# Kernel optimization log

Measured on AMD Instinct MI355X. Metric: run time of the kernel, lower is better.

Reference implementation:

```python
import jax, jax.numpy as jnp
import numpy as np

K = 5  # spline kernel size per pseudo-coordinate dim (dim=2 -> 25 weight matrices)


def spline_conv(x, pseudo, W, root, bias, tails, heads):
    # x: [N, Cin], pseudo: [E, 2] in [0,1], W: [K*K, Cin, Cout], root: [Cin, Cout], bias: [Cout]
    # Degree-1 open B-spline basis: each dim contributes 2 taps -> 4 (basis, weight-index) pairs per edge.
    N = x.shape[0]
    v = pseudo * (K - 1)                         # [E, 2]
    f = jnp.minimum(jnp.floor(v), K - 2)         # clamp so idx+1 <= K-1 (pseudo==1 edge case)
    frac = v - f                                 # [E, 2]
    fi = f.astype(jnp.int32)
    # Precompute per-node transform under every kernel bin: Z[n, k, :] = x[n] @ W[k]
    Z = jnp.einsum('ni,kio->nko', x, W)          # [N, 25, Cout]
    msg = jnp.zeros((pseudo.shape[0], W.shape[2]), x.dtype)
    for s in range(4):                           # 4 basis combos (static small loop)
        b0, b1 = s & 1, (s >> 1) & 1
        basis = (frac[:, 0] if b0 else 1.0 - frac[:, 0]) * (frac[:, 1] if b1 else 1.0 - frac[:, 1])
        wi = (fi[:, 0] + b0) + (fi[:, 1] + b1) * K   # [E] flattened kernel index
        msg = msg + basis[:, None] * Z[tails, wi]    # gather transformed source feature
    agg = jax.ops.segment_max(msg, heads, num_segments=N)  # scatter-max at target nodes
    agg = jnp.where(jnp.isfinite(agg), agg, 0.0)            # empty segments -> 0 (torch_scatter semantics)
    return agg + x @ root + bias


def setup_inputs() -> dict:
    N, E, D = 4096, 65536, 1024
    key = jax.random.key(0)
    ks = jax.random.split(key, 12)
    descs = jax.random.normal(ks[0], (N, D), dtype=jnp.float32)
    pts = jax.random.uniform(ks[1], (N, 2), dtype=jnp.float32) * 256.0  # keypoint coords, rescale=256 in source
    tails = jax.random.randint(ks[2], (E,), 0, N)
    heads = jax.random.randint(ks[3], (E,), 0, N)
    W1 = jax.random.normal(ks[4], (K * K, D, D), dtype=jnp.float32) * 0.02
    root1 = jax.random.normal(ks[5], (D, D), dtype=jnp.float32) * 0.03
    bias1 = jnp.zeros((D,), dtype=jnp.float32)
    W2 = jax.random.normal(ks[6], (K * K, D, D), dtype=jnp.float32) * 0.02
    root2 = jax.random.normal(ks[7], (D, D), dtype=jnp.float32) * 0.03
    bias2 = jnp.zeros((D,), dtype=jnp.float32)
    return {"descs": descs, "pts": pts, "W1": W1, "root1": root1, "bias1": bias1,
            "W2": W2, "root2": root2, "bias2": bias2, "tails": tails, "heads": heads}


def reference(descs, pts, W1, root1, bias1, W2, root2, bias2, tails, heads):
    # Edge pseudo-coordinates: 0.5*(pts[tail]-pts[head])/256 + 0.5, clipped to [0,1] (Net.to_pyg_graph)
    pseudo = jnp.clip(0.5 * (pts[tails] - pts[heads]) / 256.0 + 0.5, 0.0, 1.0)
    # SConv: relu(conv1) -> conv2, then residual x + 0.1*result (SiameseSConvOnNodes)
    h1 = jax.nn.relu(spline_conv(descs, pseudo, W1, root1, bias1, tails, heads))
    h2 = spline_conv(h1, pseudo, W2, root2, bias2, tails, heads)
    return descs + 0.1 * h2
```

## Files before the change

### kernel.cpp

```cpp
#include <hip/hip_runtime.h>
#include <hip/hip_bf16.h>
#include <math.h>


#define DN 4096
#define DE 65536
#define DF 1024
#define NMAT 26
#define NCOLS (NMAT * DF)

typedef __attribute__((ext_vector_type(8))) short short8;
typedef __attribute__((ext_vector_type(4))) float f32x4;
typedef unsigned long long ull;

__device__ __forceinline__ float bf2f(unsigned short u) {
    return __uint_as_float(((unsigned int)u) << 16);
}
__device__ __forceinline__ unsigned short f2bf(float f) {
    unsigned int x = __float_as_uint(f);
    x += 0x7fffu + ((x >> 16) & 1u);
    return (unsigned short)(x >> 16);
}
__device__ __forceinline__ void gld16(const unsigned short* g, unsigned short* l) {
    __builtin_amdgcn_global_load_lds(
        (const __attribute__((address_space(1))) unsigned int*)g,
        (__attribute__((address_space(3))) unsigned int*)l, 16, 0, 0);
}

__global__ void k_convert_x(const float* __restrict__ x, unsigned short* __restrict__ xb) {
    int i = (blockIdx.x * blockDim.x + threadIdx.x) * 4;
    float4 v = *(const float4*)(x + i);
    union { unsigned short u[4]; ull ll; } o;
    o.u[0] = f2bf(v.x); o.u[1] = f2bf(v.y); o.u[2] = f2bf(v.z); o.u[3] = f2bf(v.w);
    *(ull*)(xb + i) = o.ll;
}

__global__ void k_hist(const int* __restrict__ heads, int* __restrict__ cnt) {
    int e = blockIdx.x * blockDim.x + threadIdx.x;
    atomicAdd(&cnt[heads[e]], 1);
}

__global__ __launch_bounds__(1024)
void k_scan(const int* __restrict__ cnt, int* __restrict__ row_off, int* __restrict__ cursor) {
    __shared__ int part[1024];
    int tid = threadIdx.x;
    int base = tid * 4;
    int v[4], s = 0;
#pragma unroll
    for (int j = 0; j < 4; ++j) { v[j] = s; s += cnt[base + j]; }
    part[tid] = s;
    __syncthreads();
    for (int off = 1; off < 1024; off <<= 1) {
        int t = (tid >= off) ? part[tid - off] : 0;
        __syncthreads();
        part[tid] += t;
        __syncthreads();
    }
    int excl = (tid == 0) ? 0 : part[tid - 1];
#pragma unroll
    for (int j = 0; j < 4; ++j) {
        row_off[base + j] = excl + v[j];
        cursor[base + j]  = excl + v[j];
    }
    if (tid == 1023) row_off[4096] = part[1023];
}

__global__ void k_scatter(const float* __restrict__ pts,
                          const int* __restrict__ tails, const int* __restrict__ heads,
                          int* __restrict__ cursor,
                          int2* __restrict__ ei, float4* __restrict__ eb) {
    int e = blockIdx.x * blockDim.x + threadIdx.x;
    int t = tails[e], h = heads[e];
    float ptx = pts[2 * t], pty = pts[2 * t + 1];
    float phx = pts[2 * h], phy = pts[2 * h + 1];
    float p0 = fminf(fmaxf((ptx - phx) * (0.5f / 256.f) + 0.5f, 0.f), 1.f);
    float p1 = fminf(fmaxf((pty - phy) * (0.5f / 256.f) + 0.5f, 0.f), 1.f);
    float v0 = p0 * 4.f, v1 = p1 * 4.f;
    float f0 = fminf(floorf(v0), 3.f), f1 = fminf(floorf(v1), 3.f);
    float fr0 = v0 - f0, fr1 = v1 - f1;
    int i0 = (int)f0, i1 = (int)f1;
    int wi0 = i0 + i1 * 5;
    int wi1 = wi0 + 1;
    int wi2 = wi0 + 5;
    int wi3 = wi0 + 6;
    float4 b;
    b.x = (1.f - fr0) * (1.f - fr1);
    b.y = fr0 * (1.f - fr1);
    b.z = (1.f - fr0) * fr1;
    b.w = fr0 * fr1;
    int pos = atomicAdd(&cursor[h], 1);
    ei[pos] = make_int2(t, wi0 | (wi1 << 8) | (wi2 << 16) | (wi3 << 24));
    eb[pos] = b;
}

__global__ void k_transpose_w(const float* __restrict__ W, const float* __restrict__ root,
                              unsigned short* __restrict__ Wbt) {
    __shared__ float tile[64][65];
    int mat = blockIdx.z;
    const float* src = (mat < 25) ? (W + (size_t)mat * DF * DF) : root;
    unsigned short* dst = Wbt + (size_t)mat * DF * DF;
    int i0 = blockIdx.x * 64;
    int o0 = blockIdx.y * 64;
    int tx = threadIdx.x & 63, ty = threadIdx.x >> 6;
#pragma unroll
    for (int j = 0; j < 16; ++j) {
        int r = j * 4 + ty;
        tile[r][tx] = src[(size_t)(i0 + r) * DF + o0 + tx];
    }
    __syncthreads();
#pragma unroll
    for (int j = 0; j < 16; ++j) {
        int c = j * 4 + ty;
        dst[(size_t)(o0 + c) * DF + i0 + tx] = f2bf(tile[tx][c]);
    }
}

__global__ __launch_bounds__(256)
void k_gemm(const unsigned short* __restrict__ A,
            const unsigned short* __restrict__ B,
            unsigned short* __restrict__ C)
{
    __shared__ unsigned short As[128 * 32];
    __shared__ unsigned short Bs[128 * 32];
    const int tid = threadIdx.x;
    const int w = tid >> 6, ln = tid & 63;
    const int wr = w >> 1, wc = w & 1;
    const int bm = blockIdx.x, bn = blockIdx.y;

    f32x4 acc[4][4];
#pragma unroll
    for (int m = 0; m < 4; ++m)
#pragma unroll
        for (int n = 0; n < 4; ++n) acc[m][n] = (f32x4){0.f, 0.f, 0.f, 0.f};

    const size_t abase = (size_t)bm * 128 * 1024;
    const size_t bbase = (size_t)bn * 128 * 1024;
    const int k0 = (ln >> 4) * 8;
    const int rsel = ln & 15;

    for (int kk = 0; kk < 32; ++kk) {
        const int kbase = kk * 32;
#pragma unroll
        for (int j = 0; j < 2; ++j) {
            int chunk = j * 4 + w;
            int byteoff = chunk * 1024 + ln * 16;
            int row = byteoff >> 6;
            int ke = (byteoff & 63) >> 1;
            gld16(A + abase + (size_t)row * 1024 + kbase + ke, &As[chunk * 512]);
            gld16(B + bbase + (size_t)row * 1024 + kbase + ke, &Bs[chunk * 512]);
        }
        __syncthreads();
        short8 af[4], bf[4];
#pragma unroll
        for (int m = 0; m < 4; ++m)
            af[m] = *(const short8*)&As[(wr * 64 + m * 16 + rsel) * 32 + k0];
#pragma unroll
        for (int n = 0; n < 4; ++n)
            bf[n] = *(const short8*)&Bs[(wc * 64 + n * 16 + rsel) * 32 + k0];
#pragma unroll
        for (int m = 0; m < 4; ++m)
#pragma unroll
            for (int n = 0; n < 4; ++n)
                acc[m][n] = __builtin_amdgcn_mfma_f32_16x16x32_bf16(af[m], bf[n], acc[m][n], 0, 0, 0);
        __syncthreads();
    }

    const int r0 = (ln >> 4) * 4;
#pragma unroll
    for (int m = 0; m < 4; ++m) {
#pragma unroll
        for (int n = 0; n < 4; ++n) {
            int row = bm * 128 + wr * 64 + m * 16 + r0;
            int col = bn * 128 + wc * 64 + n * 16 + (ln & 15);
#pragma unroll
            for (int r = 0; r < 4; ++r)
                C[(size_t)(row + r) * NCOLS + col] = f2bf(acc[m][n][r]);
        }
    }
}

template <int LAYER>
__global__ __launch_bounds__(256)
void k_agg(const int* __restrict__ row_off,
           const int2* __restrict__ ei, const float4* __restrict__ eb,
           const unsigned short* __restrict__ Z,
           const float* __restrict__ bias,
           const float* __restrict__ descs,
           unsigned short* __restrict__ h1b, float* __restrict__ out)
{
    __shared__ int2  sei[64];
    __shared__ float4 seb[64];
    const int n = blockIdx.x;
    const int tid = threadIdx.x;
    const int d = tid * 4;
    const int s0 = row_off[n], s1 = row_off[n + 1];

    float vm0 = -3.3e38f, vm1 = -3.3e38f, vm2 = -3.3e38f, vm3 = -3.3e38f;

    for (int chunk = s0; chunk < s1; chunk += 64) {
        int cnum = min(64, s1 - chunk);
        if (tid < cnum) { sei[tid] = ei[chunk + tid]; seb[tid] = eb[chunk + tid]; }
        __syncthreads();
        for (int j = 0; j < cnum; ++j) {
            int2 ep = sei[j];
            float4 b = seb[j];
            const unsigned short* zt = Z + (size_t)ep.x * NCOLS + d;
            int w = ep.y;
            ull q0 = *(const ull*)(zt + ((w      ) & 255) * DF);
            ull q1 = *(const ull*)(zt + ((w >> 8 ) & 255) * DF);
            ull q2 = *(const ull*)(zt + ((w >> 16) & 255) * DF);
            ull q3 = *(const ull*)(zt + ((w >> 24) & 255) * DF);
            float m0 = b.x * bf2f((unsigned short)q0) + b.y * bf2f((unsigned short)q1)
                     + b.z * bf2f((unsigned short)q2) + b.w * bf2f((unsigned short)q3);
            float m1 = b.x * bf2f((unsigned short)(q0 >> 16)) + b.y * bf2f((unsigned short)(q1 >> 16))
                     + b.z * bf2f((unsigned short)(q2 >> 16)) + b.w * bf2f((unsigned short)(q3 >> 16));
            float m2 = b.x * bf2f((unsigned short)(q0 >> 32)) + b.y * bf2f((unsigned short)(q1 >> 32))
                     + b.z * bf2f((unsigned short)(q2 >> 32)) + b.w * bf2f((unsigned short)(q3 >> 32));
            float m3 = b.x * bf2f((unsigned short)(q0 >> 48)) + b.y * bf2f((unsigned short)(q1 >> 48))
                     + b.z * bf2f((unsigned short)(q2 >> 48)) + b.w * bf2f((unsigned short)(q3 >> 48));
            vm0 = fmaxf(vm0, m0); vm1 = fmaxf(vm1, m1);
            vm2 = fmaxf(vm2, m2); vm3 = fmaxf(vm3, m3);
        }
        __syncthreads();
    }
    if (s1 == s0) { vm0 = vm1 = vm2 = vm3 = 0.f; }

    const unsigned short* zr = Z + (size_t)n * NCOLS + 25 * DF + d;
    ull qr = *(const ull*)zr;
    float z0 = bf2f((unsigned short)qr),         z1 = bf2f((unsigned short)(qr >> 16));
    float z2 = bf2f((unsigned short)(qr >> 32)), z3 = bf2f((unsigned short)(qr >> 48));
    float b0 = bias[d], b1 = bias[d + 1], b2 = bias[d + 2], b3 = bias[d + 3];
    size_t o = (size_t)n * DF + d;
    if (LAYER == 1) {
        union { unsigned short u[4]; ull ll; } ov;
        ov.u[0] = f2bf(fmaxf(vm0 + z0 + b0, 0.f));
        ov.u[1] = f2bf(fmaxf(vm1 + z1 + b1, 0.f));
        ov.u[2] = f2bf(fmaxf(vm2 + z2 + b2, 0.f));
        ov.u[3] = f2bf(fmaxf(vm3 + z3 + b3, 0.f));
        *(ull*)(h1b + o) = ov.ll;
    } else {
        float4 dv = *(const float4*)(descs + o);
        float4 r;
        r.x = dv.x + 0.1f * (vm0 + z0 + b0);
        r.y = dv.y + 0.1f * (vm1 + z1 + b1);
        r.z = dv.z + 0.1f * (vm2 + z2 + b2);
        r.w = dv.w + 0.1f * (vm3 + z3 + b3);
        *(float4*)(out + o) = r;
    }
}

extern "C" void kernel_launch(void* const* d_in, const int* in_sizes, int n_in,
                              void* d_out, int out_size, void* d_ws, size_t ws_size,
                              hipStream_t stream) {
    const float* descs = (const float*)d_in[0];
    const float* pts   = (const float*)d_in[1];
    const float* W1    = (const float*)d_in[2];
    const float* root1 = (const float*)d_in[3];
    const float* bias1 = (const float*)d_in[4];
    const float* W2    = (const float*)d_in[5];
    const float* root2 = (const float*)d_in[6];
    const float* bias2 = (const float*)d_in[7];
    const int* tails   = (const int*)d_in[8];
    const int* heads   = (const int*)d_in[9];
    float* out = (float*)d_out;

    char* ws = (char*)d_ws;
    unsigned short* Wbt = (unsigned short*)ws;  ws += (size_t)NMAT * DF * DF * 2;
    unsigned short* xb  = (unsigned short*)ws;  ws += (size_t)DN * DF * 2;
    unsigned short* h1b = (unsigned short*)ws;  ws += (size_t)DN * DF * 2;
    unsigned short* Z   = (unsigned short*)ws;  ws += (size_t)DN * NCOLS * 2;
    int*  cnt     = (int*)ws;   ws += DN * 4;
    int*  row_off = (int*)ws;   ws += (DN + 1) * 4 + 4;
    int*  cursor  = (int*)ws;   ws += DN * 4;
    int2* ei      = (int2*)ws;  ws += (size_t)DE * 8;
    float4* eb    = (float4*)ws; ws += (size_t)DE * 16;

    hipMemsetAsync(cnt, 0, DN * 4, stream);
    k_convert_x<<<DN * DF / 4 / 256, 256, 0, stream>>>(descs, xb);
    k_hist<<<DE / 256, 256, 0, stream>>>(heads, cnt);
    k_scan<<<1, 1024, 0, stream>>>(cnt, row_off, cursor);
    k_scatter<<<DE / 256, 256, 0, stream>>>(pts, tails, heads, cursor, ei, eb);

    k_transpose_w<<<dim3(16, 16, NMAT), 256, 0, stream>>>(W1, root1, Wbt);
    k_gemm<<<dim3(DN / 128, NCOLS / 128), 256, 0, stream>>>(xb, Wbt, Z);
    k_agg<1><<<DN, 256, 0, stream>>>(row_off, ei, eb, Z, bias1, nullptr, h1b, nullptr);

    k_transpose_w<<<dim3(16, 16, NMAT), 256, 0, stream>>>(W2, root2, Wbt);
    k_gemm<<<dim3(DN / 128, NCOLS / 128), 256, 0, stream>>>(h1b, Wbt, Z);
    k_agg<2><<<DN, 256, 0, stream>>>(row_off, ei, eb, Z, bias2, descs, nullptr, out);
}
```

Measured before the change: 942.5 us.

## Rewrite GEMM with 256x128 tiles, triple-buffered LDS, XOR swizzle and block remap

The GEMM kernel moves to 512-thread blocks computing 256x128 tiles with a K-step of 64. Global-to-LDS loads are triple-buffered and issued two stages ahead, with split waitcnt/barrier phases and s_setprio around the MFMA blocks. LDS rows are XOR-swizzled to avoid bank conflicts, and workgroup IDs are remapped in groups of 8 for L2 locality. The goal is to hide global load latency and raise MFMA utilisation in the dominant projection GEMM, at the cost of more LDS per block (144KB across two blocks) and tighter, fragile hand-tuned synchronisation.

```diff
diff --git a/kernel.cpp b/kernel.cpp
--- a/kernel.cpp
+++ b/kernel.cpp
@@ -80,16 +80,13 @@
     float fr0 = v0 - f0, fr1 = v1 - f1;
     int i0 = (int)f0, i1 = (int)f1;
     int wi0 = i0 + i1 * 5;
-    int wi1 = wi0 + 1;
-    int wi2 = wi0 + 5;
-    int wi3 = wi0 + 6;
     float4 b;
     b.x = (1.f - fr0) * (1.f - fr1);
     b.y = fr0 * (1.f - fr1);
     b.z = (1.f - fr0) * fr1;
     b.w = fr0 * fr1;
     int pos = atomicAdd(&cursor[h], 1);
-    ei[pos] = make_int2(t, wi0 | (wi1 << 8) | (wi2 << 16) | (wi3 << 24));
+    ei[pos] = make_int2(t, wi0 | ((wi0 + 1) << 8) | ((wi0 + 5) << 16) | ((wi0 + 6) << 24));
     eb[pos] = b;
 }
 
@@ -115,17 +112,34 @@
     }
 }
 
-__global__ __launch_bounds__(256)
+__global__ __launch_bounds__(512, 2)
 void k_gemm(const unsigned short* __restrict__ A,
             const unsigned short* __restrict__ B,
             unsigned short* __restrict__ C)
 {
-    __shared__ unsigned short As[128 * 32];
-    __shared__ unsigned short Bs[128 * 32];
+    __shared__ unsigned short As[3][16384];
+    __shared__ unsigned short Bs[3][8192];
+
     const int tid = threadIdx.x;
-    const int w = tid >> 6, ln = tid & 63;
-    const int wr = w >> 1, wc = w & 1;
-    const int bm = blockIdx.x, bn = blockIdx.y;
+    const int w  = tid >> 6, ln = tid & 63;
+    const int wr = w >> 1,  wc = w & 1;
+
+    int wg  = blockIdx.x;
+    int swz = (wg & 7) * 416 + (wg >> 3);
+    int bm  = swz / 208, bn = swz - bm * 208;
+
+    const size_t abase = (size_t)bm * 256 * 1024;
+    const size_t bbase = (size_t)bn * 128 * 1024;
+
+    const int lrow = ln >> 3;
+    const int lswz = ((ln & 7) ^ lrow) * 8;
+
+#define STAGE_A(l, kt, b) \
+    gld16(A + abase + (size_t)((l) * 64 + w * 8 + lrow) * 1024 + (size_t)(kt) * 64 + lswz, \
+          &As[b][(l) * 4096 + w * 512]);
+#define STAGE_B(l, kt, b) \
+    gld16(B + bbase + (size_t)((l) * 64 + w * 8 + lrow) * 1024 + (size_t)(kt) * 64 + lswz, \
+          &Bs[b][(l) * 4096 + w * 512]);
 
     f32x4 acc[4][4];
 #pragma unroll
@@ -133,44 +147,73 @@
 #pragma unroll
         for (int n = 0; n < 4; ++n) acc[m][n] = (f32x4){0.f, 0.f, 0.f, 0.f};
 
-    const size_t abase = (size_t)bm * 128 * 1024;
-    const size_t bbase = (size_t)bn * 128 * 1024;
-    const int k0 = (ln >> 4) * 8;
-    const int rsel = ln & 15;
-
-    for (int kk = 0; kk < 32; ++kk) {
-        const int kbase = kk * 32;
-#pragma unroll
-        for (int j = 0; j < 2; ++j) {
-            int chunk = j * 4 + w;
-            int byteoff = chunk * 1024 + ln * 16;
-            int row = byteoff >> 6;
-            int ke = (byteoff & 63) >> 1;
-            gld16(A + abase + (size_t)row * 1024 + kbase + ke, &As[chunk * 512]);
-            gld16(B + bbase + (size_t)row * 1024 + kbase + ke, &Bs[chunk * 512]);
-        }
-        __syncthreads();
+    const int rsel  = ln & 15, klane = ln >> 4;
+    const int sl0   = ((klane ^ (rsel & 7)) * 8);
+    const int sl1   = sl0 ^ 32;
+    int arow[4], brow[4];
+#pragma unroll
+    for (int m = 0; m < 4; ++m) arow[m] = (wr * 64 + m * 16 + rsel) * 64;
+#pragma unroll
+    for (int n = 0; n < 4; ++n) brow[n] = (wc * 64 + n * 16 + rsel) * 64;
+
+    STAGE_A(0, 0, 0) STAGE_A(1, 0, 0) STAGE_A(2, 0, 0) STAGE_A(3, 0, 0)
+    STAGE_B(0, 0, 0) STAGE_B(1, 0, 0)
+    STAGE_A(0, 1, 1) STAGE_A(1, 1, 1) STAGE_A(2, 1, 1) STAGE_A(3, 1, 1)
+    STAGE_B(0, 1, 1) STAGE_B(1, 1, 1)
+    asm volatile("s_waitcnt vmcnt(6)" ::: "memory");
+    __builtin_amdgcn_s_barrier();
+
+    int cb = 0;
+#pragma unroll 1
+    for (int t = 0; t < 16; ++t) {
+        int sb = cb + 2; if (sb >= 3) sb -= 3;
+        const unsigned short* Ab = &As[cb][0];
+        const unsigned short* Bb = &Bs[cb][0];
+        const bool st = (t + 2) < 16;
+
         short8 af[4], bf[4];
 #pragma unroll
-        for (int m = 0; m < 4; ++m)
-            af[m] = *(const short8*)&As[(wr * 64 + m * 16 + rsel) * 32 + k0];
-#pragma unroll
-        for (int n = 0; n < 4; ++n)
-            bf[n] = *(const short8*)&Bs[(wc * 64 + n * 16 + rsel) * 32 + k0];
+        for (int m = 0; m < 4; ++m) af[m] = *(const short8*)&Ab[arow[m] + sl0];
+#pragma unroll
+        for (int n = 0; n < 4; ++n) bf[n] = *(const short8*)&Bb[brow[n] + sl0];
+        if (st) { STAGE_A(0, t + 2, sb) STAGE_A(1, t + 2, sb) STAGE_A(2, t + 2, sb) }
+        __builtin_amdgcn_s_barrier();
+        __builtin_amdgcn_s_setprio(1);
 #pragma unroll
         for (int m = 0; m < 4; ++m)
 #pragma unroll
             for (int n = 0; n < 4; ++n)
                 acc[m][n] = __builtin_amdgcn_mfma_f32_16x16x32_bf16(af[m], bf[n], acc[m][n], 0, 0, 0);
-        __syncthreads();
-    }
+        __builtin_amdgcn_s_setprio(0);
+        __builtin_amdgcn_s_barrier();
+
+#pragma unroll
+        for (int m = 0; m < 4; ++m) af[m] = *(const short8*)&Ab[arow[m] + sl1];
+#pragma unroll
+        for (int n = 0; n < 4; ++n) bf[n] = *(const short8*)&Bb[brow[n] + sl1];
+        if (st) { STAGE_A(3, t + 2, sb) STAGE_B(0, t + 2, sb) STAGE_B(1, t + 2, sb) }
+        __builtin_amdgcn_s_barrier();
+        __builtin_amdgcn_s_setprio(1);
+#pragma unroll
+        for (int m = 0; m < 4; ++m)
+#pragma unroll
+            for (int n = 0; n < 4; ++n)
+                acc[m][n] = __builtin_amdgcn_mfma_f32_16x16x32_bf16(af[m], bf[n], acc[m][n], 0, 0, 0);
+        __builtin_amdgcn_s_setprio(0);
+        if (t < 14)       { asm volatile("s_waitcnt vmcnt(6)" ::: "memory"); }
+        else if (t == 14) { asm volatile("s_waitcnt vmcnt(0)" ::: "memory"); }
+        __builtin_amdgcn_s_barrier();
+        cb = cb + 1; if (cb >= 3) cb = 0;
+    }
+#undef STAGE_A
+#undef STAGE_B
 
     const int r0 = (ln >> 4) * 4;
 #pragma unroll
     for (int m = 0; m < 4; ++m) {
 #pragma unroll
         for (int n = 0; n < 4; ++n) {
-            int row = bm * 128 + wr * 64 + m * 16 + r0;
+            int row = bm * 256 + wr * 64 + m * 16 + r0;
             int col = bn * 128 + wc * 64 + n * 16 + (ln & 15);
 #pragma unroll
             for (int r = 0; r < 4; ++r)
@@ -282,10 +325,10 @@
     k_scatter<<<DE / 256, 256, 0, stream>>>(pts, tails, heads, cursor, ei, eb);
 
     k_transpose_w<<<dim3(16, 16, NMAT), 256, 0, stream>>>(W1, root1, Wbt);
-    k_gemm<<<dim3(DN / 128, NCOLS / 128), 256, 0, stream>>>(xb, Wbt, Z);
+    k_gemm<<<(DN / 256) * (NCOLS / 128), 512, 0, stream>>>(xb, Wbt, Z);
     k_agg<1><<<DN, 256, 0, stream>>>(row_off, ei, eb, Z, bias1, nullptr, h1b, nullptr);
 
     k_transpose_w<<<dim3(16, 16, NMAT), 256, 0, stream>>>(W2, root2, Wbt);
-    k_gemm<<<dim3(DN / 128, NCOLS / 128), 256, 0, stream>>>(h1b, Wbt, Z);
+    k_gemm<<<(DN / 256) * (NCOLS / 128), 512, 0, stream>>>(h1b, Wbt, Z);
     k_agg<2><<<DN, 256, 0, stream>>>(row_off, ei, eb, Z, bias2, descs, nullptr, out);
 }
```

Measured after the change: 945.6 us. No clear change (+0.3%).
